# Kernel tuning notes

Hardware: AMD Instinct MI355X
Metric: run time of the kernel (lower is better)

The kernel has to match this reference:

```python
import jax, jax.numpy as jnp
import numpy as np

NUM_LAYERS = 4
NUM_HEADS = 8
D_MODEL = 256
D_FF = 1024
UNC_THRESHOLD = 0.3
B, L = 2, 2048


def _layer_norm(x, g, b, eps=1e-5):
    m = jnp.mean(x, axis=-1, keepdims=True)
    v = jnp.mean((x - m) ** 2, axis=-1, keepdims=True)
    return (x - m) * jax.lax.rsqrt(v + eps) * g + b


def setup_inputs() -> dict:
    key = jax.random.key(0)
    ks = jax.random.split(key, 32)
    D, F, Ly = D_MODEL, D_FF, NUM_LAYERS
    w = lambda k, shape: jax.random.normal(k, shape, dtype=jnp.float32) * 0.02
    return {
        'x': jax.random.normal(ks[0], (B, L, D), dtype=jnp.float32),
        'Win': w(ks[1], (D, D)), 'bin_': jnp.zeros((D,), jnp.float32),
        'Wq': w(ks[2], (Ly, D, D)), 'bq': jnp.zeros((Ly, D), jnp.float32),
        'Wk': w(ks[3], (Ly, D, D)), 'bk': jnp.zeros((Ly, D), jnp.float32),
        'Wv': w(ks[4], (Ly, D, D)), 'bv': jnp.zeros((Ly, D), jnp.float32),
        'Wo': w(ks[5], (Ly, D, D)), 'bo': jnp.zeros((Ly, D), jnp.float32),
        'ev_scale': jnp.ones((Ly,), jnp.float32),
        'ev_bias': jnp.zeros((Ly,), jnp.float32),
        'W1': w(ks[6], (Ly, D, F)), 'b1': jnp.zeros((Ly, F), jnp.float32),
        'W2': w(ks[7], (Ly, F, D)), 'b2': jnp.zeros((Ly, D), jnp.float32),
        'n1g': jnp.ones((Ly, D), jnp.float32), 'n1b': jnp.zeros((Ly, D), jnp.float32),
        'n2g': jnp.ones((Ly, D), jnp.float32), 'n2b': jnp.zeros((Ly, D), jnp.float32),
        'fng': jnp.ones((D,), jnp.float32), 'fnb': jnp.zeros((D,), jnp.float32),
        'Wout': w(ks[8], (D, D)), 'bout': jnp.zeros((D,), jnp.float32),
    }


def _evidence_attention(x, Wq, bq, Wk, bk, Wv, bv, Wo, bo, scale, bias):
    b, l, d = x.shape
    hd = d // NUM_HEADS
    def heads(t):
        return t.reshape(b, l, NUM_HEADS, hd).transpose(0, 2, 1, 3)  # [B,H,L,hd]
    Q = heads(x @ Wq + bq)
    K = heads(x @ Wk + bk)
    V = heads(x @ Wv + bv)
    scores = jnp.einsum('bhqd,bhkd->bhqk', Q, K) / np.sqrt(hd).astype(np.float32)
    evidence = jnp.exp(scores) * scale + 1.0 + bias           # [B,H,L,L]
    denom = jnp.sum(evidence, axis=-1, keepdims=True)         # [B,H,L,1]
    uncertainty = (jnp.float32(l) / denom)[..., 0]            # [B,H,L]
    probs = evidence / denom
    attn = jnp.einsum('bhqk,bhkd->bhqd', probs, V)
    attn = attn.transpose(0, 2, 1, 3).reshape(b, l, d)
    return attn @ Wo + bo, uncertainty


def reference(x, Win, bin_, Wq, bq, Wk, bk, Wv, bv, Wo, bo, ev_scale, ev_bias,
              W1, b1, W2, b2, n1g, n1b, n2g, n2b, fng, fnb, Wout, bout):
    h = x @ Win + bin_
    total_unc = 0.0
    for i in range(NUM_LAYERS):
        attn_out, unc = _evidence_attention(
            _layer_norm(h, n1g[i], n1b[i]),
            Wq[i], bq[i], Wk[i], bk[i], Wv[i], bv[i], Wo[i], bo[i],
            ev_scale[i], ev_bias[i])
        h = h + attn_out
        ff = jax.nn.gelu(_layer_norm(h, n2g[i], n2b[i]) @ W1[i] + b1[i], approximate=False) @ W2[i] + b2[i]
        h = h + ff
        total_unc = total_unc + unc
    avg_unc = total_unc / NUM_LAYERS                          # [B,H,L]
    out = _layer_norm(h, fng, fnb) @ Wout + bout              # [B,L,D]
    should_abstain = avg_unc > UNC_THRESHOLD
    return out, avg_unc, should_abstain
```

## Files before the change

kernel.cpp:

```cpp
#include <hip/hip_runtime.h>
#include <hip/hip_bf16.h>
#include <math.h>

#define B_  2
#define L_  2048
#define D_  256
#define H_  8
#define HD_ 32
#define F_  1024
#define LY_ 4
#define M_  (B_*L_)

typedef __attribute__((ext_vector_type(8))) short bf16x8;
typedef __attribute__((ext_vector_type(4))) float f32x4;

static __device__ __forceinline__ short f2bf(float f) {
    return __builtin_bit_cast(short, __float2bfloat16(f));
}

static __device__ __forceinline__ void gload_lds16(const ushort* g, ushort* l) {
    __builtin_amdgcn_global_load_lds(
        (const __attribute__((address_space(1))) void*)g,
        (__attribute__((address_space(3))) void*)l, 16, 0, 0);
}

__global__ __launch_bounds__(256) void transpose_weights(
    const float* __restrict__ Win, const float* __restrict__ Wq,
    const float* __restrict__ Wk,  const float* __restrict__ Wv,
    const float* __restrict__ Wo,  const float* __restrict__ W1,
    const float* __restrict__ W2,  const float* __restrict__ Wout,
    ushort* __restrict__ T)
{
    const int bid = blockIdx.x;
    const float* src; ushort* dst; int K, N, tt;
    if (bid < 64)        { src = Win; dst = T; K = 256; N = 256; tt = bid; }
    else if (bid < 1088) {
        int i = bid - 64; int which = i >> 8; int l = (i >> 6) & 3; tt = i & 63;
        K = 256; N = 256;
        const float* s4[4] = {Wq, Wk, Wv, Wo};
        src = s4[which] + l * 65536;
        dst = T + 65536 * (1 + which * 4 + l);
    } else if (bid < 2112) {
        int i = bid - 1088; int l = i >> 8; tt = i & 255; K = 256; N = 1024;
        src = W1 + l * 262144; dst = T + 65536 * 17 + l * 262144;
    } else if (bid < 3136) {
        int i = bid - 2112; int l = i >> 8; tt = i & 255; K = 1024; N = 256;
        src = W2 + l * 262144; dst = T + 65536 * 17 + 1048576 + l * 262144;
    } else {
        src = Wout; dst = T + 65536 * 17 + 2097152; K = 256; N = 256; tt = bid - 3136;
    }
    const int ntn = N >> 5;
    const int tk = tt / ntn, tn = tt % ntn;
    __shared__ float ld[32][33];
    const int t = threadIdx.x;
    const int r = t >> 3, c4 = (t & 7) * 4;
    float4 v = *reinterpret_cast<const float4*>(&src[(size_t)(tk * 32 + r) * N + tn * 32 + c4]);
    ld[r][c4 + 0] = v.x; ld[r][c4 + 1] = v.y; ld[r][c4 + 2] = v.z; ld[r][c4 + 3] = v.w;
    __syncthreads();
    short4 o;
    o.x = f2bf(ld[c4 + 0][r]);
    o.y = f2bf(ld[c4 + 1][r]);
    o.z = f2bf(ld[c4 + 2][r]);
    o.w = f2bf(ld[c4 + 3][r]);
    *reinterpret_cast<short4*>(&dst[(size_t)(tn * 32 + r) * K + tk * 32 + c4]) = o;
}

__global__ __launch_bounds__(256) void f32_to_bf16(
    const float* __restrict__ in, ushort* __restrict__ out)
{
    const int i = (blockIdx.x * 256 + threadIdx.x) * 4;
    float4 v = *reinterpret_cast<const float4*>(&in[i]);
    short4 o = {f2bf(v.x), f2bf(v.y), f2bf(v.z), f2bf(v.w)};
    *reinterpret_cast<short4*>(&out[i]) = o;
}

__device__ __forceinline__ void gemm_core64(
    const ushort* __restrict__ A, const ushort* __restrict__ Wt, int K,
    int row0, int col0, ushort* sA, ushort* sW, f32x4 acc[2][2])
{
    const int tid  = threadIdx.x;
    const int lane = tid & 63;
    const int wid  = tid >> 6;
    const int wr = wid >> 1, wc = wid & 1;
    const int g = lane >> 4, nn = lane & 15;

    const int r0 = tid >> 3;
    const int sx = ((tid & 7) ^ (r0 & 7)) << 3;

    const ushort* Ap = &A[(size_t)(row0 + r0) * K + sx];
    const ushort* Wp = &Wt[(size_t)(col0 + r0) * K + sx];
    const size_t rstep = (size_t)32 * K;

    ushort* ldsA = sA + wid * 512;
    ushort* ldsW = sW + wid * 512;

    gload_lds16(Ap,         ldsA);
    gload_lds16(Ap + rstep, ldsA + 2048);
    gload_lds16(Wp,         ldsW);
    gload_lds16(Wp + rstep, ldsW + 2048);

    const int ra = (wr * 32 + nn) * 64, rb = ra + 16 * 64;
    const int rc = (wc * 32 + nn) * 64, rd = rc + 16 * 64;
    const int m7 = nn & 7;

    int cur = 0;
    __syncthreads();
    for (int k0 = 0; k0 < K; k0 += 64) {
        if (k0 + 64 < K) {
            ushort* lA = ldsA + (cur ^ 1) * 4096;
            ushort* lW = ldsW + (cur ^ 1) * 4096;
            gload_lds16(Ap + k0 + 64,         lA);
            gload_lds16(Ap + k0 + 64 + rstep, lA + 2048);
            gload_lds16(Wp + k0 + 64,         lW);
            gload_lds16(Wp + k0 + 64 + rstep, lW + 2048);
        }
        const ushort* a = sA + cur * 4096;
        const ushort* w = sW + cur * 4096;
#pragma unroll
        for (int sk = 0; sk < 2; ++sk) {
            const int sw = ((sk * 4 + g) ^ m7) << 3;
            bf16x8 a0 = *reinterpret_cast<const bf16x8*>(&a[ra + sw]);
            bf16x8 a1 = *reinterpret_cast<const bf16x8*>(&a[rb + sw]);
            bf16x8 w0 = *reinterpret_cast<const bf16x8*>(&w[rc + sw]);
            bf16x8 w1 = *reinterpret_cast<const bf16x8*>(&w[rd + sw]);
            acc[0][0] = __builtin_amdgcn_mfma_f32_16x16x32_bf16(a0, w0, acc[0][0], 0, 0, 0);
            acc[0][1] = __builtin_amdgcn_mfma_f32_16x16x32_bf16(a0, w1, acc[0][1], 0, 0, 0);
            acc[1][0] = __builtin_amdgcn_mfma_f32_16x16x32_bf16(a1, w0, acc[1][0], 0, 0, 0);
            acc[1][1] = __builtin_amdgcn_mfma_f32_16x16x32_bf16(a1, w1, acc[1][1], 0, 0, 0);
        }
        __syncthreads();
        cur ^= 1;
    }
}

template<int EPI, int OUTBF>
__global__ __launch_bounds__(256) void gemm_bf16(
    const ushort* __restrict__ A, const ushort* __restrict__ Wt,
    const float* __restrict__ bias, const float* __restrict__ res,
    void* __restrict__ Cout, int M, int N, int K)
{
    __shared__ __align__(16) ushort sA[2 * 4096];
    __shared__ __align__(16) ushort sW[2 * 4096];
    const int row0 = blockIdx.y * 64, col0 = blockIdx.x * 64;
    f32x4 acc[2][2] = {};
    gemm_core64(A, Wt, K, row0, col0, sA, sW, acc);

    const int lane = threadIdx.x & 63;
    const int wid  = threadIdx.x >> 6;
    const int wr = wid >> 1, wc = wid & 1;
    const int g = lane >> 4, nn = lane & 15;
#pragma unroll
    for (int mi = 0; mi < 2; ++mi)
#pragma unroll
    for (int ni = 0; ni < 2; ++ni)
#pragma unroll
    for (int r = 0; r < 4; ++r) {
        const int m = row0 + wr * 32 + mi * 16 + g * 4 + r;
        const int c = col0 + wc * 32 + ni * 16 + nn;
        float v = acc[mi][ni][r] + bias[c];
        if (EPI == 1) v = 0.5f * v * (1.0f + erff(v * 0.70710678118654752f));
        if (EPI == 2) v += res[(size_t)m * N + c];
        if (OUTBF) ((ushort*)Cout)[(size_t)m * N + c] = (ushort)f2bf(v);
        else       ((float*)Cout)[(size_t)m * N + c] = v;
    }
}

__global__ __launch_bounds__(256) void gemm_qkv(
    const ushort* __restrict__ A,
    const ushort* __restrict__ WqT, const ushort* __restrict__ WkT,
    const ushort* __restrict__ WvT,
    const float* __restrict__ bq, const float* __restrict__ bk,
    const float* __restrict__ bv,
    ushort* __restrict__ Qb, ushort* __restrict__ Kb, ushort* __restrict__ Vt)
{
    __shared__ __align__(16) ushort sA[2 * 4096];
    __shared__ __align__(16) ushort sW[2 * 4096];
    const int nb = blockIdx.x;
    const int wsel = nb >> 2;
    const int col0 = (nb & 3) * 64;
    const int row0 = blockIdx.y * 64;
    const ushort* Wt = (wsel == 0) ? WqT : (wsel == 1) ? WkT : WvT;
    const float* bias = (wsel == 0) ? bq : (wsel == 1) ? bk : bv;

    f32x4 acc[2][2] = {};
    gemm_core64(A, Wt, 256, row0, col0, sA, sW, acc);

    const int lane = threadIdx.x & 63;
    const int wid  = threadIdx.x >> 6;
    const int wr = wid >> 1, wc = wid & 1;
    const int g = lane >> 4, nn = lane & 15;
    ushort* QK = (wsel == 0) ? Qb : Kb;
#pragma unroll
    for (int mi = 0; mi < 2; ++mi)
#pragma unroll
    for (int ni = 0; ni < 2; ++ni)
#pragma unroll
    for (int r = 0; r < 4; ++r) {
        const int m = row0 + wr * 32 + mi * 16 + g * 4 + r;
        const int c = col0 + wc * 32 + ni * 16 + nn;
        const float v = acc[mi][ni][r] + bias[c];
        if (wsel < 2) {
            QK[(size_t)m * D_ + c] = (ushort)f2bf(v);
        } else {
            const int b = m >> 11, l = m & 2047;
            const int h = c >> 5,  d = c & 31;
            Vt[(size_t)((b * 8 + h) * 32 + d) * L_ + l] = (ushort)f2bf(v);
        }
    }
}

__global__ __launch_bounds__(256) void ln_kernel(
    const float* __restrict__ x, const float* __restrict__ g,
    const float* __restrict__ b, ushort* __restrict__ y)
{
    const int row = blockIdx.x;
    const int tid = threadIdx.x;
    const float v = x[row * D_ + tid];
    float s = v, s2 = v * v;
#pragma unroll
    for (int off = 32; off > 0; off >>= 1) {
        s  += __shfl_xor(s,  off);
        s2 += __shfl_xor(s2, off);
    }
    __shared__ float ls[4], ls2[4];
    const int wid = tid >> 6;
    if ((tid & 63) == 0) { ls[wid] = s; ls2[wid] = s2; }
    __syncthreads();
    s  = ls[0]  + ls[1]  + ls[2]  + ls[3];
    s2 = ls2[0] + ls2[1] + ls2[2] + ls2[3];
    const float m   = s * (1.0f / D_);
    const float var = s2 * (1.0f / D_) - m * m;
    const float r   = rsqrtf(var + 1e-5f);
    y[row * D_ + tid] = (ushort)f2bf((v - m) * r * g[tid] + b[tid]);
}

__global__ __launch_bounds__(256) void attn_mfma(
    const ushort* __restrict__ Qb, const ushort* __restrict__ Kb,
    const ushort* __restrict__ Vt, ushort* __restrict__ O,
    float* __restrict__ unc, const float* __restrict__ ev_scale,
    const float* __restrict__ ev_bias, int layer)
{
    const int bh = blockIdx.y;
    const int b  = bh >> 3;
    const int h  = bh & 7;
    const int tid  = threadIdx.x;
    const int wv   = tid >> 6;
    const int lane = tid & 63;
    const int g = lane >> 4;
    const int n = lane & 15;
    const int q  = blockIdx.x * 64 + wv * 16 + n;
    const float scale = ev_scale[layer];
    const float cb    = 1.0f + ev_bias[layer];
    const float isq   = 0.17677669529663687f;

    __shared__ __align__(16) ushort sK[2][64][40];
    __shared__ __align__(16) ushort sV[2][32][72];

    const size_t qk0 = (size_t)b * L_ * D_ + h * HD_;

    bf16x8 qf;
    {
        const bf16x8 qr = *reinterpret_cast<const bf16x8*>(&Qb[qk0 + (size_t)q * D_ + g * 8]);
#pragma unroll
        for (int j = 0; j < 8; ++j) {
            const float qv = __builtin_bit_cast(float, ((unsigned)(unsigned short)qr[j]) << 16);
            qf[j] = f2bf(qv * isq);
        }
    }
    bf16x8 ones;
#pragma unroll
    for (int j = 0; j < 8; ++j) ones[j] = (short)0x3F80;

    const int krow = tid >> 2, kch = (tid & 3) * 8;
    const int vrow = tid >> 3, vch = (tid & 7) * 8;
    const ushort* ksrc = Kb + qk0 + (size_t)krow * D_ + kch;
    const ushort* vsrc = Vt + (size_t)((b * 8 + h) * 32 + vrow) * L_ + vch;

    f32x4 acc0 = {0.f, 0.f, 0.f, 0.f};
    f32x4 acc1 = {0.f, 0.f, 0.f, 0.f};
    f32x4 accS = {0.f, 0.f, 0.f, 0.f};
    const f32x4 zero = {0.f, 0.f, 0.f, 0.f};

    bf16x8 kreg = *reinterpret_cast<const bf16x8*>(ksrc);
    bf16x8 vreg = *reinterpret_cast<const bf16x8*>(vsrc);

    int cur = 0;
    for (int t = 0; t < L_; t += 64) {
        *reinterpret_cast<bf16x8*>(&sK[cur][krow][kch]) = kreg;
        *reinterpret_cast<bf16x8*>(&sV[cur][vrow][vch]) = vreg;
        if (t + 64 < L_) {
            kreg = *reinterpret_cast<const bf16x8*>(ksrc + (size_t)(t + 64) * D_);
            vreg = *reinterpret_cast<const bf16x8*>(vsrc + (t + 64));
        }
        __syncthreads();

#pragma unroll
        for (int tt = 0; tt < 64; tt += 32) {
            bf16x8 kf0 = *reinterpret_cast<const bf16x8*>(&sK[cur][tt + n][g * 8]);
            bf16x8 kf1 = *reinterpret_cast<const bf16x8*>(&sK[cur][tt + 16 + n][g * 8]);

            f32x4 s0 = __builtin_amdgcn_mfma_f32_16x16x32_bf16(kf0, qf, zero, 0, 0, 0);
            f32x4 s1 = __builtin_amdgcn_mfma_f32_16x16x32_bf16(kf1, qf, zero, 0, 0, 0);

            short4 va = *reinterpret_cast<const short4*>(&sV[cur][n][tt + g * 4]);
            short4 vb = *reinterpret_cast<const short4*>(&sV[cur][n][tt + 16 + g * 4]);
            short4 vc = *reinterpret_cast<const short4*>(&sV[cur][n + 16][tt + g * 4]);
            short4 vd = *reinterpret_cast<const short4*>(&sV[cur][n + 16][tt + 16 + g * 4]);
            bf16x8 vf0 = {va.x, va.y, va.z, va.w, vb.x, vb.y, vb.z, vb.w};
            bf16x8 vf1 = {vc.x, vc.y, vc.z, vc.w, vd.x, vd.y, vd.z, vd.w};

            bf16x8 pa;
#pragma unroll
            for (int r = 0; r < 4; ++r) pa[r]     = f2bf(fmaf(__expf(s0[r]), scale, cb));
#pragma unroll
            for (int r = 0; r < 4; ++r) pa[r + 4] = f2bf(fmaf(__expf(s1[r]), scale, cb));

            acc0 = __builtin_amdgcn_mfma_f32_16x16x32_bf16(vf0, pa, acc0, 0, 0, 0);
            acc1 = __builtin_amdgcn_mfma_f32_16x16x32_bf16(vf1, pa, acc1, 0, 0, 0);
            accS = __builtin_amdgcn_mfma_f32_16x16x32_bf16(ones, pa, accS, 0, 0, 0);
        }
        cur ^= 1;
    }

    const float inv = 1.0f / accS[0];

    ushort* op = &O[qk0 + (size_t)q * D_ + g * 4];
    short4 o0 = {f2bf(acc0[0] * inv), f2bf(acc0[1] * inv), f2bf(acc0[2] * inv), f2bf(acc0[3] * inv)};
    short4 o1 = {f2bf(acc1[0] * inv), f2bf(acc1[1] * inv), f2bf(acc1[2] * inv), f2bf(acc1[3] * inv)};
    *reinterpret_cast<short4*>(op)      = o0;
    *reinterpret_cast<short4*>(op + 16) = o1;

    if (g == 0) {
        const float u = (float)L_ * inv;
        const int uidx = bh * L_ + q;
        unc[uidx] = (layer == 0) ? u : (unc[uidx] + u);
    }
}

__global__ __launch_bounds__(256) void unc_final(
    const float* __restrict__ unc, float* __restrict__ out_unc,
    float* __restrict__ out_abst)
{
    const int i = blockIdx.x * 256 + threadIdx.x;
    const float u = unc[i] * 0.25f;
    out_unc[i]  = u;
    out_abst[i] = (u > 0.3f) ? 1.0f : 0.0f;
}

extern "C" void kernel_launch(void* const* d_in, const int* in_sizes, int n_in,
                              void* d_out, int out_size, void* d_ws, size_t ws_size,
                              hipStream_t stream)
{
    const float* x    = (const float*)d_in[0];
    const float* Win  = (const float*)d_in[1];
    const float* bin_ = (const float*)d_in[2];
    const float* Wq   = (const float*)d_in[3];
    const float* bq   = (const float*)d_in[4];
    const float* Wk   = (const float*)d_in[5];
    const float* bk   = (const float*)d_in[6];
    const float* Wv   = (const float*)d_in[7];
    const float* bv   = (const float*)d_in[8];
    const float* Wo   = (const float*)d_in[9];
    const float* bo   = (const float*)d_in[10];
    const float* evs  = (const float*)d_in[11];
    const float* evb  = (const float*)d_in[12];
    const float* W1   = (const float*)d_in[13];
    const float* b1   = (const float*)d_in[14];
    const float* W2   = (const float*)d_in[15];
    const float* b2   = (const float*)d_in[16];
    const float* n1g  = (const float*)d_in[17];
    const float* n1b  = (const float*)d_in[18];
    const float* n2g  = (const float*)d_in[19];
    const float* n2b  = (const float*)d_in[20];
    const float* fng  = (const float*)d_in[21];
    const float* fnb  = (const float*)d_in[22];
    const float* Wout = (const float*)d_in[23];
    const float* bout = (const float*)d_in[24];

    char* ws = (char*)d_ws;
    float*  h    = (float*) (ws);
    ushort* tmpb = (ushort*)(ws + (4  << 20));
    ushort* Qb   = (ushort*)(ws + (6  << 20));
    ushort* Kb   = (ushort*)(ws + (8  << 20));
    ushort* Vt   = (ushort*)(ws + (10 << 20));
    ushort* Ob   = (ushort*)(ws + (12 << 20));
    ushort* ffb  = (ushort*)(ws + (6  << 20));
    float*  unc  = (float*) (ws + (14 << 20));
    ushort* T    = (ushort*)(ws + (15 << 20));

    ushort* winT  = T;
    ushort* woutT = T + 65536 * 17 + 2097152;

    float* out_main = (float*)d_out;
    float* out_unc  = out_main + M_ * D_;
    float* out_abst = out_unc + B_ * H_ * L_;

    const dim3 blk(256);
    const dim3 g256(4, 64);
    const dim3 g1024(16, 64);
    const dim3 gqkv(12, 64);
    const dim3 gattn(L_ / 64, B_ * H_);

    transpose_weights<<<3200, blk, 0, stream>>>(Win, Wq, Wk, Wv, Wo, W1, W2, Wout, T);
    f32_to_bf16<<<1024, blk, 0, stream>>>(x, tmpb);
    gemm_bf16<0, 0><<<g256, blk, 0, stream>>>(tmpb, winT, bin_, nullptr, h, M_, D_, D_);

    for (int i = 0; i < LY_; ++i) {
        ushort* wqT = T + 65536 * (1 + i);
        ushort* wkT = T + 65536 * (5 + i);
        ushort* wvT = T + 65536 * (9 + i);
        ushort* woT = T + 65536 * (13 + i);
        ushort* w1T = T + 65536 * 17 + i * 262144;
        ushort* w2T = T + 65536 * 17 + 1048576 + i * 262144;

        ln_kernel<<<M_, blk, 0, stream>>>(h, n1g + i * D_, n1b + i * D_, tmpb);
        gemm_qkv<<<gqkv, blk, 0, stream>>>(tmpb, wqT, wkT, wvT,
                                           bq + i * D_, bk + i * D_, bv + i * D_,
                                           Qb, Kb, Vt);
        attn_mfma<<<gattn, blk, 0, stream>>>(Qb, Kb, Vt, Ob, unc, evs, evb, i);
        gemm_bf16<2, 0><<<g256, blk, 0, stream>>>(Ob, woT, bo + i * D_, h, h, M_, D_, D_);
        ln_kernel<<<M_, blk, 0, stream>>>(h, n2g + i * D_, n2b + i * D_, tmpb);
        gemm_bf16<1, 1><<<g1024, blk, 0, stream>>>(tmpb, w1T, b1 + i * F_, nullptr, ffb, M_, F_, D_);
        gemm_bf16<2, 0><<<g256, blk, 0, stream>>>(ffb, w2T, b2 + i * D_, h, h, M_, D_, F_);
    }

    ln_kernel<<<M_, blk, 0, stream>>>(h, fng, fnb, tmpb);
    gemm_bf16<0, 0><<<g256, blk, 0, stream>>>(tmpb, woutT, bout, nullptr, out_main, M_, D_, D_);
    unc_final<<<(B_ * H_ * L_) / 256, blk, 0, stream>>>(unc, out_unc, out_abst);
}
```

Measured before the change: 301.5 us.

## Fuse LayerNorm into following GEMM prologues and fold uncertainty finalization into attention

Layer norm (and the initial fp32-to-bf16 cast) is now computed inside the GEMM blocks. Each block loads 64 full rows of h, normalizes them into LDS, and streams only the weights through double buffers. The separate ln_kernel, f32_to_bf16 and unc_final launches go away, with the last layer's attention pass writing the averaged uncertainty and abstain flags directly. This removes several launches and the bf16 intermediate round-trips, but the LN work is repeated by every column block (16x for the FFN up-projection), and the larger LDS footprint may reduce occupancy.

```diff
diff --git a/kernel.cpp b/kernel.cpp
--- a/kernel.cpp
+++ b/kernel.cpp
@@ -65,13 +65,170 @@
     *reinterpret_cast<short4*>(&dst[(size_t)(tn * 32 + r) * K + tk * 32 + c4]) = o;
 }
 
-__global__ __launch_bounds__(256) void f32_to_bf16(
-    const float* __restrict__ in, ushort* __restrict__ out)
-{
-    const int i = (blockIdx.x * 256 + threadIdx.x) * 4;
-    float4 v = *reinterpret_cast<const float4*>(&in[i]);
-    short4 o = {f2bf(v.x), f2bf(v.y), f2bf(v.z), f2bf(v.w)};
-    *reinterpret_cast<short4*>(&out[i]) = o;
+template<int LNMODE>
+__device__ __forceinline__ void gemm_core_ln(
+    const float* __restrict__ Hin, const float* __restrict__ lng,
+    const float* __restrict__ lnb, const ushort* __restrict__ Wt,
+    int row0, int col0, ushort* sLN, ushort* sW, f32x4 acc[2][2])
+{
+    const int tid  = threadIdx.x;
+    const int lane = tid & 63;
+    const int wid  = tid >> 6;
+    const int wr = wid >> 1, wc = wid & 1;
+    const int g = lane >> 4, nn = lane & 15;
+
+    const int r0 = tid >> 3;
+    const int sx = ((tid & 7) ^ (r0 & 7)) << 3;
+    const ushort* Wp = &Wt[(size_t)(col0 + r0) * 256 + sx];
+    ushort* ldsW = sW + wid * 512;
+    gload_lds16(Wp,            ldsW);
+    gload_lds16(Wp + 32 * 256, ldsW + 2048);
+
+    {
+        const int prow = tid >> 2;
+        const int pq   = tid & 3;
+        const float* hp = &Hin[(size_t)(row0 + prow) * D_ + pq * 64];
+        float4 v[16];
+#pragma unroll
+        for (int j = 0; j < 16; ++j) v[j] = reinterpret_cast<const float4*>(hp)[j];
+        float mean = 0.f, rstd = 0.f;
+        if (LNMODE) {
+            float s = 0.f, s2 = 0.f;
+#pragma unroll
+            for (int j = 0; j < 16; ++j) {
+                s  += v[j].x + v[j].y + v[j].z + v[j].w;
+                s2 += v[j].x * v[j].x + v[j].y * v[j].y + v[j].z * v[j].z + v[j].w * v[j].w;
+            }
+            s  += __shfl_xor(s, 1);  s  += __shfl_xor(s, 2);
+            s2 += __shfl_xor(s2, 1); s2 += __shfl_xor(s2, 2);
+            mean = s * (1.0f / D_);
+            const float var = s2 * (1.0f / D_) - mean * mean;
+            rstd = rsqrtf(var + 1e-5f);
+        }
+        ushort* dst = &sLN[prow * 264 + pq * 64];
+#pragma unroll
+        for (int j = 0; j < 16; ++j) {
+            short4 o;
+            if (LNMODE) {
+                const int c = pq * 64 + j * 4;
+                o.x = f2bf((v[j].x - mean) * rstd * lng[c + 0] + lnb[c + 0]);
+                o.y = f2bf((v[j].y - mean) * rstd * lng[c + 1] + lnb[c + 1]);
+                o.z = f2bf((v[j].z - mean) * rstd * lng[c + 2] + lnb[c + 2]);
+                o.w = f2bf((v[j].w - mean) * rstd * lng[c + 3] + lnb[c + 3]);
+            } else {
+                o.x = f2bf(v[j].x); o.y = f2bf(v[j].y);
+                o.z = f2bf(v[j].z); o.w = f2bf(v[j].w);
+            }
+            *reinterpret_cast<short4*>(dst + j * 4) = o;
+        }
+    }
+
+    const int ra = (wr * 32 + nn) * 264, rb = ra + 16 * 264;
+    const int rc = (wc * 32 + nn) * 64,  rd = rc + 16 * 64;
+    const int m7 = nn & 7;
+
+    int cur = 0;
+    __syncthreads();
+#pragma unroll
+    for (int k0 = 0; k0 < 256; k0 += 64) {
+        if (k0 + 64 < 256) {
+            ushort* lW = ldsW + (cur ^ 1) * 4096;
+            gload_lds16(Wp + k0 + 64,            lW);
+            gload_lds16(Wp + k0 + 64 + 32 * 256, lW + 2048);
+        }
+        const ushort* w = sW + cur * 4096;
+#pragma unroll
+        for (int sk = 0; sk < 2; ++sk) {
+            const int ac = k0 + sk * 32 + g * 8;
+            bf16x8 a0 = *reinterpret_cast<const bf16x8*>(&sLN[ra + ac]);
+            bf16x8 a1 = *reinterpret_cast<const bf16x8*>(&sLN[rb + ac]);
+            const int sw = ((sk * 4 + g) ^ m7) << 3;
+            bf16x8 w0 = *reinterpret_cast<const bf16x8*>(&w[rc + sw]);
+            bf16x8 w1 = *reinterpret_cast<const bf16x8*>(&w[rd + sw]);
+            acc[0][0] = __builtin_amdgcn_mfma_f32_16x16x32_bf16(a0, w0, acc[0][0], 0, 0, 0);
+            acc[0][1] = __builtin_amdgcn_mfma_f32_16x16x32_bf16(a0, w1, acc[0][1], 0, 0, 0);
+            acc[1][0] = __builtin_amdgcn_mfma_f32_16x16x32_bf16(a1, w0, acc[1][0], 0, 0, 0);
+            acc[1][1] = __builtin_amdgcn_mfma_f32_16x16x32_bf16(a1, w1, acc[1][1], 0, 0, 0);
+        }
+        __syncthreads();
+        cur ^= 1;
+    }
+}
+
+template<int LNMODE, int EPI, int OUTBF>
+__global__ __launch_bounds__(256) void gemm_ln(
+    const float* __restrict__ Hin, const float* __restrict__ lng,
+    const float* __restrict__ lnb, const ushort* __restrict__ Wt,
+    const float* __restrict__ bias, void* __restrict__ Cout, int N)
+{
+    __shared__ __align__(16) ushort sLN[64 * 264];
+    __shared__ __align__(16) ushort sW[2 * 4096];
+    const int row0 = blockIdx.y * 64, col0 = blockIdx.x * 64;
+    f32x4 acc[2][2] = {};
+    gemm_core_ln<LNMODE>(Hin, lng, lnb, Wt, row0, col0, sLN, sW, acc);
+
+    const int lane = threadIdx.x & 63;
+    const int wid  = threadIdx.x >> 6;
+    const int wr = wid >> 1, wc = wid & 1;
+    const int g = lane >> 4, nn = lane & 15;
+#pragma unroll
+    for (int mi = 0; mi < 2; ++mi)
+#pragma unroll
+    for (int ni = 0; ni < 2; ++ni)
+#pragma unroll
+    for (int r = 0; r < 4; ++r) {
+        const int m = row0 + wr * 32 + mi * 16 + g * 4 + r;
+        const int c = col0 + wc * 32 + ni * 16 + nn;
+        float v = acc[mi][ni][r] + bias[c];
+        if (EPI == 1) v = 0.5f * v * (1.0f + erff(v * 0.70710678118654752f));
+        if (OUTBF) ((ushort*)Cout)[(size_t)m * N + c] = (ushort)f2bf(v);
+        else       ((float*)Cout)[(size_t)m * N + c] = v;
+    }
+}
+
+__global__ __launch_bounds__(256) void gemm_qkv_ln(
+    const float* __restrict__ Hin, const float* __restrict__ lng,
+    const float* __restrict__ lnb,
+    const ushort* __restrict__ WqT, const ushort* __restrict__ WkT,
+    const ushort* __restrict__ WvT,
+    const float* __restrict__ bq, const float* __restrict__ bk,
+    const float* __restrict__ bv,
+    ushort* __restrict__ Qb, ushort* __restrict__ Kb, ushort* __restrict__ Vt)
+{
+    __shared__ __align__(16) ushort sLN[64 * 264];
+    __shared__ __align__(16) ushort sW[2 * 4096];
+    const int nb = blockIdx.x;
+    const int wsel = nb >> 2;
+    const int col0 = (nb & 3) * 64;
+    const int row0 = blockIdx.y * 64;
+    const ushort* Wt = (wsel == 0) ? WqT : (wsel == 1) ? WkT : WvT;
+    const float* bias = (wsel == 0) ? bq : (wsel == 1) ? bk : bv;
+
+    f32x4 acc[2][2] = {};
+    gemm_core_ln<1>(Hin, lng, lnb, Wt, row0, col0, sLN, sW, acc);
+
+    const int lane = threadIdx.x & 63;
+    const int wid  = threadIdx.x >> 6;
+    const int wr = wid >> 1, wc = wid & 1;
+    const int g = lane >> 4, nn = lane & 15;
+    ushort* QK = (wsel == 0) ? Qb : Kb;
+#pragma unroll
+    for (int mi = 0; mi < 2; ++mi)
+#pragma unroll
+    for (int ni = 0; ni < 2; ++ni)
+#pragma unroll
+    for (int r = 0; r < 4; ++r) {
+        const int m = row0 + wr * 32 + mi * 16 + g * 4 + r;
+        const int c = col0 + wc * 32 + ni * 16 + nn;
+        const float v = acc[mi][ni][r] + bias[c];
+        if (wsel < 2) {
+            QK[(size_t)m * D_ + c] = (ushort)f2bf(v);
+        } else {
+            const int b = m >> 11, l = m & 2047;
+            const int h = c >> 5,  d = c & 31;
+            Vt[(size_t)((b * 8 + h) * 32 + d) * L_ + l] = (ushort)f2bf(v);
+        }
+    }
 }
 
 __device__ __forceinline__ void gemm_core64(
@@ -133,11 +290,9 @@
     }
 }
 
-template<int EPI, int OUTBF>
-__global__ __launch_bounds__(256) void gemm_bf16(
+__global__ __launch_bounds__(256) void gemm_res(
     const ushort* __restrict__ A, const ushort* __restrict__ Wt,
-    const float* __restrict__ bias, const float* __restrict__ res,
-    void* __restrict__ Cout, int M, int N, int K)
+    const float* __restrict__ bias, float* __restrict__ C, int K)
 {
     __shared__ __align__(16) ushort sA[2 * 4096];
     __shared__ __align__(16) ushort sW[2 * 4096];
@@ -157,88 +312,16 @@
     for (int r = 0; r < 4; ++r) {
         const int m = row0 + wr * 32 + mi * 16 + g * 4 + r;
         const int c = col0 + wc * 32 + ni * 16 + nn;
-        float v = acc[mi][ni][r] + bias[c];
-        if (EPI == 1) v = 0.5f * v * (1.0f + erff(v * 0.70710678118654752f));
-        if (EPI == 2) v += res[(size_t)m * N + c];
-        if (OUTBF) ((ushort*)Cout)[(size_t)m * N + c] = (ushort)f2bf(v);
-        else       ((float*)Cout)[(size_t)m * N + c] = v;
-    }
-}
-
-__global__ __launch_bounds__(256) void gemm_qkv(
-    const ushort* __restrict__ A,
-    const ushort* __restrict__ WqT, const ushort* __restrict__ WkT,
-    const ushort* __restrict__ WvT,
-    const float* __restrict__ bq, const float* __restrict__ bk,
-    const float* __restrict__ bv,
-    ushort* __restrict__ Qb, ushort* __restrict__ Kb, ushort* __restrict__ Vt)
-{
-    __shared__ __align__(16) ushort sA[2 * 4096];
-    __shared__ __align__(16) ushort sW[2 * 4096];
-    const int nb = blockIdx.x;
-    const int wsel = nb >> 2;
-    const int col0 = (nb & 3) * 64;
-    const int row0 = blockIdx.y * 64;
-    const ushort* Wt = (wsel == 0) ? WqT : (wsel == 1) ? WkT : WvT;
-    const float* bias = (wsel == 0) ? bq : (wsel == 1) ? bk : bv;
-
-    f32x4 acc[2][2] = {};
-    gemm_core64(A, Wt, 256, row0, col0, sA, sW, acc);
-
-    const int lane = threadIdx.x & 63;
-    const int wid  = threadIdx.x >> 6;
-    const int wr = wid >> 1, wc = wid & 1;
-    const int g = lane >> 4, nn = lane & 15;
-    ushort* QK = (wsel == 0) ? Qb : Kb;
-#pragma unroll
-    for (int mi = 0; mi < 2; ++mi)
-#pragma unroll
-    for (int ni = 0; ni < 2; ++ni)
-#pragma unroll
-    for (int r = 0; r < 4; ++r) {
-        const int m = row0 + wr * 32 + mi * 16 + g * 4 + r;
-        const int c = col0 + wc * 32 + ni * 16 + nn;
-        const float v = acc[mi][ni][r] + bias[c];
-        if (wsel < 2) {
-            QK[(size_t)m * D_ + c] = (ushort)f2bf(v);
-        } else {
-            const int b = m >> 11, l = m & 2047;
-            const int h = c >> 5,  d = c & 31;
-            Vt[(size_t)((b * 8 + h) * 32 + d) * L_ + l] = (ushort)f2bf(v);
-        }
-    }
-}
-
-__global__ __launch_bounds__(256) void ln_kernel(
-    const float* __restrict__ x, const float* __restrict__ g,
-    const float* __restrict__ b, ushort* __restrict__ y)
-{
-    const int row = blockIdx.x;
-    const int tid = threadIdx.x;
-    const float v = x[row * D_ + tid];
-    float s = v, s2 = v * v;
-#pragma unroll
-    for (int off = 32; off > 0; off >>= 1) {
-        s  += __shfl_xor(s,  off);
-        s2 += __shfl_xor(s2, off);
-    }
-    __shared__ float ls[4], ls2[4];
-    const int wid = tid >> 6;
-    if ((tid & 63) == 0) { ls[wid] = s; ls2[wid] = s2; }
-    __syncthreads();
-    s  = ls[0]  + ls[1]  + ls[2]  + ls[3];
-    s2 = ls2[0] + ls2[1] + ls2[2] + ls2[3];
-    const float m   = s * (1.0f / D_);
-    const float var = s2 * (1.0f / D_) - m * m;
-    const float r   = rsqrtf(var + 1e-5f);
-    y[row * D_ + tid] = (ushort)f2bf((v - m) * r * g[tid] + b[tid]);
+        C[(size_t)m * D_ + c] += acc[mi][ni][r] + bias[c];
+    }
 }
 
 __global__ __launch_bounds__(256) void attn_mfma(
     const ushort* __restrict__ Qb, const ushort* __restrict__ Kb,
     const ushort* __restrict__ Vt, ushort* __restrict__ O,
     float* __restrict__ unc, const float* __restrict__ ev_scale,
-    const float* __restrict__ ev_bias, int layer)
+    const float* __restrict__ ev_bias, int layer,
+    float* __restrict__ out_unc, float* __restrict__ out_abst)
 {
     const int bh = blockIdx.y;
     const int b  = bh >> 3;
@@ -333,18 +416,16 @@
     if (g == 0) {
         const float u = (float)L_ * inv;
         const int uidx = bh * L_ + q;
-        unc[uidx] = (layer == 0) ? u : (unc[uidx] + u);
-    }
-}
-
-__global__ __launch_bounds__(256) void unc_final(
-    const float* __restrict__ unc, float* __restrict__ out_unc,
-    float* __restrict__ out_abst)
-{
-    const int i = blockIdx.x * 256 + threadIdx.x;
-    const float u = unc[i] * 0.25f;
-    out_unc[i]  = u;
-    out_abst[i] = (u > 0.3f) ? 1.0f : 0.0f;
+        if (layer == 0) {
+            unc[uidx] = u;
+        } else if (layer < LY_ - 1) {
+            unc[uidx] += u;
+        } else {
+            const float avg = (unc[uidx] + u) * 0.25f;
+            out_unc[uidx]  = avg;
+            out_abst[uidx] = (avg > 0.3f) ? 1.0f : 0.0f;
+        }
+    }
 }
 
 extern "C" void kernel_launch(void* const* d_in, const int* in_sizes, int n_in,
@@ -379,12 +460,11 @@
 
     char* ws = (char*)d_ws;
     float*  h    = (float*) (ws);
-    ushort* tmpb = (ushort*)(ws + (4  << 20));
     ushort* Qb   = (ushort*)(ws + (6  << 20));
     ushort* Kb   = (ushort*)(ws + (8  << 20));
     ushort* Vt   = (ushort*)(ws + (10 << 20));
     ushort* Ob   = (ushort*)(ws + (12 << 20));
-    ushort* ffb  = (ushort*)(ws + (6  << 20));
+    ushort* ffb  = (ushort*)(ws + (4  << 20));
     float*  unc  = (float*) (ws + (14 << 20));
     ushort* T    = (ushort*)(ws + (15 << 20));
 
@@ -402,8 +482,7 @@
     const dim3 gattn(L_ / 64, B_ * H_);
 
     transpose_weights<<<3200, blk, 0, stream>>>(Win, Wq, Wk, Wv, Wo, W1, W2, Wout, T);
-    f32_to_bf16<<<1024, blk, 0, stream>>>(x, tmpb);
-    gemm_bf16<0, 0><<<g256, blk, 0, stream>>>(tmpb, winT, bin_, nullptr, h, M_, D_, D_);
+    gemm_ln<0, 0, 0><<<g256, blk, 0, stream>>>(x, nullptr, nullptr, winT, bin_, h, D_);
 
     for (int i = 0; i < LY_; ++i) {
         ushort* wqT = T + 65536 * (1 + i);
@@ -413,18 +492,17 @@
         ushort* w1T = T + 65536 * 17 + i * 262144;
         ushort* w2T = T + 65536 * 17 + 1048576 + i * 262144;
 
-        ln_kernel<<<M_, blk, 0, stream>>>(h, n1g + i * D_, n1b + i * D_, tmpb);
-        gemm_qkv<<<gqkv, blk, 0, stream>>>(tmpb, wqT, wkT, wvT,
-                                           bq + i * D_, bk + i * D_, bv + i * D_,
-                                           Qb, Kb, Vt);
-        attn_mfma<<<gattn, blk, 0, stream>>>(Qb, Kb, Vt, Ob, unc, evs, evb, i);
-        gemm_bf16<2, 0><<<g256, blk, 0, stream>>>(Ob, woT, bo + i * D_, h, h, M_, D_, D_);
-        ln_kernel<<<M_, blk, 0, stream>>>(h, n2g + i * D_, n2b + i * D_, tmpb);
-        gemm_bf16<1, 1><<<g1024, blk, 0, stream>>>(tmpb, w1T, b1 + i * F_, nullptr, ffb, M_, F_, D_);
-        gemm_bf16<2, 0><<<g256, blk, 0, stream>>>(ffb, w2T, b2 + i * D_, h, h, M_, D_, F_);
-    }
-
-    ln_kernel<<<M_, blk, 0, stream>>>(h, fng, fnb, tmpb);
-    gemm_bf16<0, 0><<<g256, blk, 0, stream>>>(tmpb, woutT, bout, nullptr, out_main, M_, D_, D_);
-    unc_final<<<(B_ * H_ * L_) / 256, blk, 0, stream>>>(unc, out_unc, out_abst);
-}
+        gemm_qkv_ln<<<gqkv, blk, 0, stream>>>(h, n1g + i * D_, n1b + i * D_,
+                                              wqT, wkT, wvT,
+                                              bq + i * D_, bk + i * D_, bv + i * D_,
+                                              Qb, Kb, Vt);
+        attn_mfma<<<gattn, blk, 0, stream>>>(Qb, Kb, Vt, Ob, unc, evs, evb, i,
+                                             out_unc, out_abst);
+        gemm_res<<<g256, blk, 0, stream>>>(Ob, woT, bo + i * D_, h, D_);
+        gemm_ln<1, 1, 1><<<g1024, blk, 0, stream>>>(h, n2g + i * D_, n2b + i * D_,
+                                                    w1T, b1 + i * F_, ffb, F_);
+        gemm_res<<<g256, blk, 0, stream>>>(ffb, w2T, b2 + i * D_, h, F_);
+    }
+
+    gemm_ln<1, 0, 0><<<g256, blk, 0, stream>>>(h, fng, fnb, woutT, bout, out_main, D_);
+}
```

Result: slower. 430.1 us (+42.6%).
